# Kernel tuning notes

Measured on AMD Instinct MI355X. Metric: run time of the kernel, lower is better.

The kernel has to match this reference:

```python
import jax, jax.numpy as jnp
import numpy as np

ALPHA = 0.5


def _chamfer(a, b):
    # Equivalent math to cKDTree k=1 queries: exact nearest-neighbor distances
    # between the two flattened clouds, computed brute-force.
    a = a.reshape(-1, 3)
    b = b.reshape(-1, 3)
    d2 = (jnp.sum(a * a, axis=1)[:, None]
          + jnp.sum(b * b, axis=1)[None, :]
          - 2.0 * (a @ b.T))                      # [Na, Nb]
    d = jnp.sqrt(jnp.clip(d2, 0.0))
    dist1 = jnp.min(d, axis=0)   # tree1(a).query(b): NN dist of each b point
    dist2 = jnp.min(d, axis=1)   # tree2(b).query(a): NN dist of each a point
    return jnp.mean(dist1) + jnp.mean(dist2)


def _pairwise_distances(x, y):
    # x: [B,N,3], y: [B,M,3] -> [B,N,M] euclidean distances (clamped-sqrt trick)
    x2 = jnp.sum(x * x, axis=-1, keepdims=True)            # [B,N,1]
    y2 = jnp.sum(y * y, axis=-1, keepdims=True)            # [B,M,1]
    d2 = x2 + jnp.swapaxes(y2, 2, 1) - 2.0 * jnp.einsum('bnd,bmd->bnm', x, y)
    return jnp.sqrt(jnp.clip(d2, 0.0))


def _confidence_scores(input_pcd, gt_pcd):
    # Faithful to torch.norm on the broadcast difference: [B,P,M,3] -> [B,P,M]
    diff = input_pcd[:, :, None, :] - gt_pcd[:, None, :, :]
    dist = jnp.linalg.norm(diff, axis=-1)
    min_d = jnp.min(dist, axis=-1)                         # [B,P]
    return jnp.exp(-min_d)[..., None]                      # [B,P,1]


def setup_inputs() -> dict:
    key = jax.random.key(0)
    k0, k1, k2, k3, k4 = jax.random.split(key, 5)
    B, N, M, P, NS = 4, 2048, 2048, 2048, 1024
    return {
        'pc1_0': jax.random.normal(k0, (B, N, 3), dtype=jnp.float32),
        'pc1_1': jax.random.normal(k1, (B, NS, 3), dtype=jnp.float32),
        'pc1_3': jax.random.uniform(k2, (B, P, 1), dtype=jnp.float32),
        'pc2': jax.random.normal(k3, (B, M, 3), dtype=jnp.float32),
        'pc3': jax.random.normal(k4, (B, P, 3), dtype=jnp.float32),
    }


def reference(pc1_0, pc1_1, pc1_3, pc2, pc3):
    # ChamferDistance detaches inputs in torch (cpu/numpy path) -> stop_gradient
    cd = jax.lax.stop_gradient(_chamfer(pc1_0, pc2))
    # In the original, emd_dist is immediately overwritten by pairwise_distances
    emd_dist = _pairwise_distances(pc1_0, pc2)             # [B,N,M]
    gt_scores = _confidence_scores(pc3, pc2)               # [B,P,1]
    confidence_loss = jnp.mean((pc1_3 - gt_scores) ** 2)
    seed_loss = jax.lax.stop_gradient(_chamfer(pc1_1, pc2))
    upsampling_loss = ALPHA * cd + (1.0 - ALPHA) * emd_dist
    final_loss = confidence_loss + upsampling_loss + seed_loss  # broadcasts to [B,N,M]
    return final_loss
```

## Files before the change

### kernel.cpp

```cpp
#include <hip/hip_runtime.h>
#include <math.h>


constexpr int OUT_TOTAL  = 4 * 2048 * 2048;
constexpr int PART_TOTAL = 1664 * 512;
constexpr int PART_OFS   = OUT_TOTAL - PART_TOTAL;

typedef float nfloat4 __attribute__((ext_vector_type(4)));
typedef _Float16 h2 __attribute__((ext_vector_type(2)));

static __device__ __forceinline__ float pack2h(float x, float y) {
    h2 v; v[0] = (_Float16)x; v[1] = (_Float16)y;
    return __builtin_bit_cast(float, v);
}

__global__ __launch_bounds__(256) void nn_kernel(
    const float* __restrict__ A0,
    const float* __restrict__ A1,
    const float* __restrict__ P2,
    const float* __restrict__ P3,
    float* __restrict__ part)
{
    __shared__ float4 lds[256];
    int bid = blockIdx.x;
    const float* A; const float* Bp; int at; int btile;
    if (bid < 512)       { int l = bid;        A = A0; Bp = P2; at = l >> 5; btile = l & 31; }
    else if (bid < 1024) { int l = bid - 512;  A = P2; Bp = A0; at = l >> 5; btile = l & 31; }
    else if (bid < 1280) { int l = bid - 1024; A = A1; Bp = P2; at = l >> 5; btile = l & 31; }
    else if (bid < 1536) { int l = bid - 1280; A = P2; Bp = A1; at = l >> 4; btile = l & 15; }
    else { int l = bid - 1536; int b = l >> 5; int l2 = l & 31; at = l2 >> 3; btile = l2 & 7;
           A = P3 + b * 6144; Bp = P2 + b * 6144; }

    {
        const float* s = Bp + (btile * 256 + threadIdx.x) * 3;
        float bx = s[0], by = s[1], bz = s[2];
        float nb2 = -0.5f * fmaf(bx, bx, fmaf(by, by, bz * bz));
        lds[threadIdx.x] = make_float4(pack2h(bx, by), bz, nb2, 0.f);
    }

    int a_base = at * 512 + threadIdx.x * 2;
    const float2* af = (const float2*)(A + a_base * 3);
    float2 f0 = af[0], f1 = af[1], f2 = af[2];
    float x0 = f0.x, y0 = f0.y, z0 = f1.x;
    float x1 = f1.y, y1 = f2.x, z1 = f2.y;
    float a20 = fmaf(x0, x0, fmaf(y0, y0, z0 * z0));
    float a21 = fmaf(x1, x1, fmaf(y1, y1, z1 * z1));
    h2 axy0 = __builtin_bit_cast(h2, pack2h(x0, y0));
    h2 axy1 = __builtin_bit_cast(h2, pack2h(x1, y1));
    float mx0 = -3.4e38f, mx1 = -3.4e38f;
    __syncthreads();

    #pragma unroll 4
    for (int j = 0; j < 256; j++) {
        float4 b = lds[j];
        h2 bxy = __builtin_bit_cast(h2, b.x);
        float t0 = fmaf(z0, b.y, b.z);
        float u0 = __builtin_amdgcn_fdot2(axy0, bxy, t0, false);
        mx0 = fmaxf(mx0, u0);
        float t1 = fmaf(z1, b.y, b.z);
        float u1 = __builtin_amdgcn_fdot2(axy1, bxy, t1, false);
        mx1 = fmaxf(mx1, u1);
    }
    float2 o;
    o.x = fmaxf(fmaf(-2.f, mx0, a20), 0.f);
    o.y = fmaxf(fmaf(-2.f, mx1, a21), 0.f);
    *(float2*)(part + bid * 512 + threadIdx.x * 2) = o;
}

__global__ __launch_bounds__(1024) void reduce_kernel(
    const float* __restrict__ part,
    const float* __restrict__ conf_in,
    float* __restrict__ ws)
{
    int g = blockIdx.x;
    int tid = threadIdx.x;
    int i, nb, base; float scale; bool isconf = false;
    if (g < 8)       { i = (g << 10) + tid;        base = 0    + (i >> 9) * 32; nb = 32; scale = 0.5f / 8192.f; }
    else if (g < 16) { i = ((g - 8) << 10) + tid;  base = 512  + (i >> 9) * 32; nb = 32; scale = 0.5f / 8192.f; }
    else if (g < 20) { i = ((g - 16) << 10) + tid; base = 1024 + (i >> 9) * 32; nb = 32; scale = 1.f / 4096.f; }
    else if (g < 28) { i = ((g - 20) << 10) + tid; base = 1280 + (i >> 9) * 16; nb = 16; scale = 1.f / 8192.f; }
    else             { i = ((g - 28) << 10) + tid; int b = i >> 11; int w = i & 2047;
                       base = 1536 + b * 32 + (w >> 9) * 8; nb = 8; scale = 1.f / 8192.f; isconf = true; }

    float m = 3.4e38f;
    const float* p = part + base * 512 + (i & 511);
    #pragma unroll 4
    for (int t = 0; t < nb; t++, p += 512) m = fminf(m, p[0]);
    float d = sqrtf(m);
    float sum;
    if (!isconf) {
        sum = d;
    } else {
        float e = conf_in[i] - __expf(-d);
        sum = e * e;
    }
    #pragma unroll
    for (int ofs = 32; ofs > 0; ofs >>= 1) sum += __shfl_down(sum, ofs);
    __shared__ float red[16];
    if ((tid & 63) == 0) red[tid >> 6] = sum;
    __syncthreads();
    if (tid == 0) {
        float tot = 0.f;
        #pragma unroll
        for (int i2 = 0; i2 < 16; i2++) tot += red[i2];
        ws[g] = tot * scale;
    }
}

__global__ __launch_bounds__(256) void out_kernel(
    const float* __restrict__ pc1_0,
    const float* __restrict__ pc2,
    const float* __restrict__ wsp,
    float* __restrict__ out)
{
    int blk = blockIdx.x;
    int batch = blk >> 8;
    int n8 = blk & 255;
    int tid = threadIdx.x;
    float S = 0.f;
    #pragma unroll
    for (int t = 0; t < 36; t++) S += wsp[t];
    const float* bb = pc2 + batch * 6144;
    float bx[8], by[8], bz[8];
    {
        const float4* p = (const float4*)(bb + tid * 12);
        float4 u0 = p[0], u1 = p[1], u2 = p[2];
        bx[0]=u0.x; by[0]=u0.y; bz[0]=u0.z;
        bx[1]=u0.w; by[1]=u1.x; bz[1]=u1.y;
        bx[2]=u1.z; by[2]=u1.w; bz[2]=u2.x;
        bx[3]=u2.y; by[3]=u2.z; bz[3]=u2.w;
    }
    {
        const float4* p = (const float4*)(bb + 3072 + tid * 12);
        float4 u0 = p[0], u1 = p[1], u2 = p[2];
        bx[4]=u0.x; by[4]=u0.y; bz[4]=u0.z;
        bx[5]=u0.w; by[5]=u1.x; bz[5]=u1.y;
        bx[6]=u1.z; by[6]=u1.w; bz[6]=u2.x;
        bx[7]=u2.y; by[7]=u2.z; bz[7]=u2.w;
    }
    const float* arow = pc1_0 + batch * 6144 + n8 * 24;
    float* ob = out + (long)((batch << 11) + (n8 << 3)) * 2048 + tid * 4;
    #pragma unroll
    for (int r = 0; r < 8; r++) {
        float axx = arow[r*3], ayy = arow[r*3+1], azz = arow[r*3+2];
        float o[8];
        #pragma unroll
        for (int k = 0; k < 8; k++) {
            float dx = axx - bx[k], dy = ayy - by[k], dz = azz - bz[k];
            float d2 = fmaf(dx, dx, fmaf(dy, dy, dz*dz));
            o[k] = fmaf(0.5f, sqrtf(d2), S);
        }
        nfloat4 lo = { o[0], o[1], o[2], o[3] };
        nfloat4 hi = { o[4], o[5], o[6], o[7] };
        __builtin_nontemporal_store(lo, (nfloat4*)(ob + r * 2048));
        __builtin_nontemporal_store(hi, (nfloat4*)(ob + r * 2048 + 1024));
    }
}

extern "C" void kernel_launch(void* const* d_in, const int* in_sizes, int n_in,
                              void* d_out, int out_size, void* d_ws, size_t ws_size,
                              hipStream_t stream) {
    const float* pc1_0 = (const float*)d_in[0];
    const float* pc1_1 = (const float*)d_in[1];
    const float* pc1_3 = (const float*)d_in[2];
    const float* pc2   = (const float*)d_in[3];
    const float* pc3   = (const float*)d_in[4];
    float* out = (float*)d_out;
    float* ws  = (float*)d_ws;
    float* part = out + PART_OFS;

    nn_kernel<<<1664, 256, 0, stream>>>(pc1_0, pc1_1, pc2, pc3, part);
    reduce_kernel<<<36, 1024, 0, stream>>>(part, pc1_3, ws);
    out_kernel<<<1024, 256, 0, stream>>>(pc1_0, pc2, ws, out);
}
```

Before: 114.3 us.

## Replace fp16 dot2 NN search with fp32 FMAs and 4 points per thread

The nearest-neighbour kernel drops fp16-packed xy coordinates and fdot2 in favour of full fp32 FMA distance evaluation. Each thread now processes four query points against the shared tile, with half as many threads per block, and each thread loads two candidate points into shared memory. This raises register reuse of each shared-memory read and restores fp32 accuracy. In exchange it adds ALU work per pair and lowers thread-level parallelism.

```diff
diff --git a/kernel.cpp b/kernel.cpp
--- a/kernel.cpp
+++ b/kernel.cpp
@@ -7,14 +7,8 @@
 constexpr int PART_OFS   = OUT_TOTAL - PART_TOTAL;
 
 typedef float nfloat4 __attribute__((ext_vector_type(4)));
-typedef _Float16 h2 __attribute__((ext_vector_type(2)));
 
-static __device__ __forceinline__ float pack2h(float x, float y) {
-    h2 v; v[0] = (_Float16)x; v[1] = (_Float16)y;
-    return __builtin_bit_cast(float, v);
-}
-
-__global__ __launch_bounds__(256) void nn_kernel(
+__global__ __launch_bounds__(128) void nn_kernel(
     const float* __restrict__ A0,
     const float* __restrict__ A1,
     const float* __restrict__ P2,
@@ -35,36 +29,45 @@
         const float* s = Bp + (btile * 256 + threadIdx.x) * 3;
         float bx = s[0], by = s[1], bz = s[2];
         float nb2 = -0.5f * fmaf(bx, bx, fmaf(by, by, bz * bz));
-        lds[threadIdx.x] = make_float4(pack2h(bx, by), bz, nb2, 0.f);
+        lds[threadIdx.x] = make_float4(bx, by, bz, nb2);
+        const float* s2 = Bp + (btile * 256 + 128 + threadIdx.x) * 3;
+        float cx = s2[0], cy = s2[1], cz = s2[2];
+        float nc2 = -0.5f * fmaf(cx, cx, fmaf(cy, cy, cz * cz));
+        lds[128 + threadIdx.x] = make_float4(cx, cy, cz, nc2);
     }
 
-    int a_base = at * 512 + threadIdx.x * 2;
-    const float2* af = (const float2*)(A + a_base * 3);
-    float2 f0 = af[0], f1 = af[1], f2 = af[2];
-    float x0 = f0.x, y0 = f0.y, z0 = f1.x;
-    float x1 = f1.y, y1 = f2.x, z1 = f2.y;
-    float a20 = fmaf(x0, x0, fmaf(y0, y0, z0 * z0));
-    float a21 = fmaf(x1, x1, fmaf(y1, y1, z1 * z1));
-    h2 axy0 = __builtin_bit_cast(h2, pack2h(x0, y0));
-    h2 axy1 = __builtin_bit_cast(h2, pack2h(x1, y1));
-    float mx0 = -3.4e38f, mx1 = -3.4e38f;
+    int a_base = at * 512 + threadIdx.x * 4;
+    const float4* av = (const float4*)(A + a_base * 3);
+    float4 v0 = av[0], v1 = av[1], v2 = av[2];
+    float ax[4], ay[4], az[4], a2[4], mx[4];
+    ax[0]=v0.x; ay[0]=v0.y; az[0]=v0.z;
+    ax[1]=v0.w; ay[1]=v1.x; az[1]=v1.y;
+    ax[2]=v1.z; ay[2]=v1.w; az[2]=v2.x;
+    ax[3]=v2.y; ay[3]=v2.z; az[3]=v2.w;
+    #pragma unroll
+    for (int k = 0; k < 4; k++) {
+        a2[k] = fmaf(ax[k], ax[k], fmaf(ay[k], ay[k], az[k]*az[k]));
+        mx[k] = -3.4e38f;
+    }
     __syncthreads();
 
     #pragma unroll 4
     for (int j = 0; j < 256; j++) {
         float4 b = lds[j];
-        h2 bxy = __builtin_bit_cast(h2, b.x);
-        float t0 = fmaf(z0, b.y, b.z);
-        float u0 = __builtin_amdgcn_fdot2(axy0, bxy, t0, false);
-        mx0 = fmaxf(mx0, u0);
-        float t1 = fmaf(z1, b.y, b.z);
-        float u1 = __builtin_amdgcn_fdot2(axy1, bxy, t1, false);
-        mx1 = fmaxf(mx1, u1);
+        #pragma unroll
+        for (int k = 0; k < 4; k++) {
+            float u = fmaf(az[k], b.z, b.w);
+            u = fmaf(ay[k], b.y, u);
+            u = fmaf(ax[k], b.x, u);
+            mx[k] = fmaxf(mx[k], u);
+        }
     }
-    float2 o;
-    o.x = fmaxf(fmaf(-2.f, mx0, a20), 0.f);
-    o.y = fmaxf(fmaf(-2.f, mx1, a21), 0.f);
-    *(float2*)(part + bid * 512 + threadIdx.x * 2) = o;
+    float4 o;
+    o.x = fmaxf(fmaf(-2.f, mx[0], a2[0]), 0.f);
+    o.y = fmaxf(fmaf(-2.f, mx[1], a2[1]), 0.f);
+    o.z = fmaxf(fmaf(-2.f, mx[2], a2[2]), 0.f);
+    o.w = fmaxf(fmaf(-2.f, mx[3], a2[3]), 0.f);
+    *(float4*)(part + bid * 512 + threadIdx.x * 4) = o;
 }
 
 __global__ __launch_bounds__(1024) void reduce_kernel(
@@ -169,7 +172,7 @@
     float* ws  = (float*)d_ws;
     float* part = out + PART_OFS;
 
-    nn_kernel<<<1664, 256, 0, stream>>>(pc1_0, pc1_1, pc2, pc3, part);
+    nn_kernel<<<1664, 128, 0, stream>>>(pc1_0, pc1_1, pc2, pc3, part);
     reduce_kernel<<<36, 1024, 0, stream>>>(part, pc1_3, ws);
     out_kernel<<<1024, 256, 0, stream>>>(pc1_0, pc2, ws, out);
 }
```

After: 112.3 us. About the same (-1.8%).
